# Performance work log

Hardware: AMD Instinct MI355X
Metric: run time of the kernel (lower is better)

## Reference

```python
import jax, jax.numpy as jnp
import numpy as np

B, N, C = 16, 1024, 1024
H = 16            # num_attention_heads
D = C // H        # attention_head_size = 64

def setup_inputs() -> dict:
    key = jax.random.key(0)
    k1, k2, k3 = jax.random.split(key, 3)
    scale = 1.0 / np.sqrt(C)
    return {
        "hidden_states": jax.random.normal(k1, (B, N, C), dtype=jnp.float32),
        "qkv_w": jax.random.normal(k2, (C, 3 * C), dtype=jnp.float32) * scale,
        "qkv_b": jnp.zeros((3 * C,), dtype=jnp.float32),
        "proj_w": jax.random.normal(k3, (C, C), dtype=jnp.float32) * scale,
        "proj_b": jnp.zeros((C,), dtype=jnp.float32),
    }

def reference(hidden_states, qkv_w, qkv_b, proj_w, proj_b):
    # fused QKV projection: [B, N, 3C]
    qkv = hidden_states @ qkv_w + qkv_b
    # reshape to [3, B, H, N, D]
    qkv = qkv.reshape(B, N, 3, H, D).transpose(2, 0, 3, 1, 4)
    q, k, v = qkv[0], qkv[1], qkv[2]
    # attention scores [B, H, N, N]
    scores = jnp.einsum("bhnd,bhmd->bhnm", q, k) / jnp.sqrt(jnp.float32(D))
    probs = jax.nn.softmax(scores, axis=-1)  # dropout_p=0 -> identity
    ctx = jnp.einsum("bhnm,bhmd->bhnd", probs, v)
    ctx = ctx.transpose(0, 2, 1, 3).reshape(B, N, C)
    # output projection
    return ctx @ proj_w + proj_b
```

## Files before the change

### kernel.cpp

```cpp
#include <hip/hip_runtime.h>


#define BB 16
#define NN 1024
#define CC 1024
#define HH 16
#define DD 64
#define BN (BB * NN)
#define HEADELEMS (256 * 1024 * 64)

typedef float  f4     __attribute__((ext_vector_type(4)));
typedef __bf16 bf16x8 __attribute__((ext_vector_type(8)));
typedef __bf16 bf16x4 __attribute__((ext_vector_type(4)));
typedef short  s8v    __attribute__((ext_vector_type(8)));
typedef short  s4v    __attribute__((ext_vector_type(4)));
typedef short  s2v    __attribute__((ext_vector_type(2)));

#if __has_builtin(__builtin_amdgcn_exp2f)
#define EXP2(x) __builtin_amdgcn_exp2f(x)
#else
#define EXP2(x) exp2f(x)
#endif

__device__ __forceinline__ short f2bf(float x) {
  union { float f; unsigned u; } a; a.f = x;
  unsigned r = a.u + 0x7fffu + ((a.u >> 16) & 1u);
  return (short)(r >> 16);
}

__device__ __forceinline__ void gl_lds16(const void* g, void* l) {
  __builtin_amdgcn_global_load_lds((__attribute__((address_space(1))) void*)g,
                                   (__attribute__((address_space(3))) void*)l,
                                   16, 0, 0);
}

__device__ __forceinline__ f4 mfma16(bf16x8 a, bf16x8 b, f4 c) {
  return __builtin_amdgcn_mfma_f32_16x16x32_bf16(a, b, c, 0, 0, 0);
}

__global__ void cast_bf16(const float* __restrict__ x, short* __restrict__ y) {
  int i = (blockIdx.x * 256 + threadIdx.x) * 4;
  float4 v = *(const float4*)&x[i];
  s4v o;
  o[0] = f2bf(v.x); o[1] = f2bf(v.y); o[2] = f2bf(v.z); o[3] = f2bf(v.w);
  *(s4v*)&y[i] = o;
}

__global__ void transpose_cast(const float* __restrict__ W, short* __restrict__ Wt,
                               int K, int Nw) {
  __shared__ float tile[32][33];
  int bx = blockIdx.x, by = blockIdx.y;
  int t = threadIdx.x;
  int tc = t & 31, tr = t >> 5;
#pragma unroll
  for (int i = 0; i < 4; ++i) {
    int r = tr + i * 8;
    tile[r][tc] = W[(size_t)(by * 32 + r) * Nw + bx * 32 + tc];
  }
  __syncthreads();
#pragma unroll
  for (int i = 0; i < 4; ++i) {
    int r = tr + i * 8;
    Wt[(size_t)(bx * 32 + r) * K + by * 32 + tc] = f2bf(tile[tc][r]);
  }
}

#define GSTAGE_A(buf, kb)                                                      \
  {                                                                            \
    _Pragma("unroll")                                                          \
    for (int rblk = 0; rblk < 4; ++rblk) {                                     \
      int rbase = (w * 4 + rblk) * 8;                                          \
      gl_lds16(A + (size_t)(row0 + rbase + sr8) * K + (kb) + sc8 * 8,          \
               &la[buf][rbase * 64]);                                          \
    }                                                                          \
  }
#define GSTAGE_B(buf, kb)                                                      \
  {                                                                            \
    _Pragma("unroll")                                                          \
    for (int bblk = 0; bblk < 2; ++bblk) {                                     \
      int rbase = (w * 2 + bblk) * 8;                                          \
      gl_lds16(Bt + (size_t)(col0 + rbase + sr8) * K + (kb) + sc8 * 8,         \
               &lb[buf][rbase * 64]);                                          \
    }                                                                          \
  }

template <int EPI>
__global__ __launch_bounds__(512, 1)
void gemm_bt(const short* __restrict__ A, const short* __restrict__ Bt,
             const float* __restrict__ bias, float* __restrict__ Cf,
             short* __restrict__ Cq, int M, int N, int K) {
  __shared__ short la[3][256 * 64];
  __shared__ short lb[2][128 * 64];
  const int t = threadIdx.x, lane = t & 63, w = t >> 6;
  int bid = blockIdx.y * gridDim.x + blockIdx.x;
  int xcd = bid & 7, sub = bid >> 3;
  int grp = sub >> 5, rem = sub & 31;
  int xb = grp * 4 + (rem & 3), yb = xcd * 8 + (rem >> 2);
  const int row0 = yb * 256, col0 = xb * 128;
  const int wm = (w >> 1) * 64, wn = (w & 1) * 64;
  const int q = lane >> 4, ln = lane & 15;
  const int sr8 = lane >> 3;
  const int sc8 = (lane & 7) ^ sr8;
  f4 acc[4][4] = {};

  const int NT = K >> 6;
  GSTAGE_A(0, 0);
  GSTAGE_B(0, 0);
  __builtin_amdgcn_sched_barrier(0);
  GSTAGE_A(1, 64);
  asm volatile("s_waitcnt vmcnt(4)" ::: "memory");
  __builtin_amdgcn_s_barrier();
  __builtin_amdgcn_sched_barrier(0);

  int curA = 0;
  for (int tt = 0; tt < NT; ++tt) {
    if (tt + 1 < NT) GSTAGE_B((tt + 1) & 1, (tt + 1) * 64);
    __builtin_amdgcn_sched_barrier(0);
    if (tt + 2 < NT) {
      int a2 = curA + 2; if (a2 >= 3) a2 -= 3;
      GSTAGE_A(a2, (tt + 2) * 64);
    }
    __builtin_amdgcn_sched_barrier(0);
#pragma unroll
    for (int ks2 = 0; ks2 < 2; ++ks2) {
      const int c8 = ks2 * 4 + q;
      const int swz = (c8 ^ (ln & 7)) * 8;
      bf16x8 af[4], bfr[4];
#pragma unroll
      for (int i = 0; i < 4; ++i) {
        af[i]  = *(const bf16x8*)&la[curA][(wm + i * 16 + ln) * 64 + swz];
        bfr[i] = *(const bf16x8*)&lb[tt & 1][(wn + i * 16 + ln) * 64 + swz];
      }
      __builtin_amdgcn_s_setprio(1);
#pragma unroll
      for (int i = 0; i < 4; ++i)
#pragma unroll
        for (int j = 0; j < 4; ++j)
          acc[i][j] = mfma16(af[i], bfr[j], acc[i][j]);
      __builtin_amdgcn_s_setprio(0);
    }
    if (tt + 2 < NT) asm volatile("s_waitcnt vmcnt(4)" ::: "memory");
    else             asm volatile("s_waitcnt vmcnt(0)" ::: "memory");
    __builtin_amdgcn_s_barrier();
    __builtin_amdgcn_sched_barrier(0);
    curA = (curA == 2) ? 0 : curA + 1;
  }

#pragma unroll
  for (int i = 0; i < 4; ++i) {
    int rbase = row0 + wm + i * 16 + q * 4;
#pragma unroll
    for (int j = 0; j < 4; ++j) {
      int col = col0 + wn + j * 16 + ln;
      float bv = bias[col];
      if (EPI == 0) {
#pragma unroll
        for (int r2 = 0; r2 < 4; ++r2)
          Cf[(size_t)(rbase + r2) * N + col] = acc[i][j][r2] + bv;
      } else {
        int which = col >> 10, c = col & 1023;
        int h = c >> 6, d = c & 63;
        if (which == 2) {
          int bh = (rbase >> 10) * HH + h;
          s4v vv;
#pragma unroll
          for (int r2 = 0; r2 < 4; ++r2) vv[r2] = f2bf(acc[i][j][r2] + bv);
          *(s4v*)&Cq[(size_t)2 * HEADELEMS + ((size_t)bh * DD + d) * NN + (rbase & 1023)] = vv;
        } else {
          float scale = (which == 0) ? 0.1803368801f : 1.0f;
#pragma unroll
          for (int r2 = 0; r2 < 4; ++r2) {
            int row = rbase + r2;
            int bh = (row >> 10) * HH + h;
            size_t idx = ((size_t)bh * NN + (row & 1023)) * DD + d;
            Cq[(size_t)which * HEADELEMS + idx] = f2bf((acc[i][j][r2] + bv) * scale);
          }
        }
      }
    }
  }
}

__global__ __launch_bounds__(512, 4)
void attn(const short* __restrict__ Qg, const short* __restrict__ Kg,
          const short* __restrict__ Vtg, short* __restrict__ ctx) {
  __shared__ short sQP[256 * 64];
  __shared__ short sK[2][64 * 64];
  __shared__ short sV[2][64 * 64];
  const int t = threadIdx.x, lane = t & 63, w = t >> 6;
  const int bh = blockIdx.x, qb = blockIdx.y;
  const short* Qh = Qg + (size_t)bh * (NN * DD) + qb * 256 * DD;
  const short* Kh = Kg + (size_t)bh * (NN * DD);
  const short* Vh = Vtg + (size_t)bh * (NN * DD);

#pragma unroll
  for (int k = 0; k < 4; ++k) {
    int i = t + k * 512;
    int r = i >> 3, c = i & 7;
    gl_lds16(Qh + r * DD + ((c ^ (r & 7)) * 8), &sQP[i * 8]);
  }
  const int sr = t >> 3, sc = t & 7;
  const int ssc = ((sc ^ (sr & 7)) * 8);
  gl_lds16(Kh + sr * DD + ssc, &sK[0][t * 8]);
  gl_lds16(Vh + (size_t)sr * NN + ssc, &sV[0][t * 8]);

  __syncthreads();

  const int q = lane >> 4, ln = lane & 15;
  const int wq = w * 32;
  const int sw = ln & 7;

  bf16x8 qf[2][2];
#pragma unroll
  for (int ks = 0; ks < 2; ++ks)
#pragma unroll
    for (int g = 0; g < 2; ++g)
      qf[ks][g] = *(const bf16x8*)&sQP[(wq + g * 16 + ln) * 64 + (((ks * 4 + q) ^ sw) * 8)];

  f4 o[2][4] = {};
  float lsum0 = 0.f, lsum1 = 0.f;

  for (int kt = 0; kt < 16; ++kt) {
    const int cur = kt & 1;
    if (kt < 15) {
      const int nb = cur ^ 1;
      gl_lds16(Kh + (kt + 1) * 64 * DD + sr * DD + ssc, &sK[nb][t * 8]);
      gl_lds16(Vh + (size_t)sr * NN + (kt + 1) * 64 + ssc, &sV[nb][t * 8]);
    }

    f4 s[4][2] = {};
    __builtin_amdgcn_s_setprio(1);
#pragma unroll
    for (int ks = 0; ks < 2; ++ks)
#pragma unroll
      for (int ki = 0; ki < 4; ++ki) {
        bf16x8 kf = *(const bf16x8*)&sK[cur][(ki * 16 + ln) * 64 + (((ks * 4 + q) ^ sw) * 8)];
        s[ki][0] = mfma16(kf, qf[ks][0], s[ki][0]);
        s[ki][1] = mfma16(kf, qf[ks][1], s[ki][1]);
      }
    __builtin_amdgcn_s_setprio(0);

#pragma unroll
    for (int g = 0; g < 2; ++g)
#pragma unroll
      for (int ki = 0; ki < 4; ++ki) {
        f4 sv = s[ki][g];
        float p0 = EXP2(sv[0]), p1 = EXP2(sv[1]);
        float p2 = EXP2(sv[2]), p3 = EXP2(sv[3]);
        if (g == 0) lsum0 += (p0 + p1) + (p2 + p3);
        else        lsum1 += (p0 + p1) + (p2 + p3);
        bf16x4 pk;
        pk[0] = (__bf16)p0; pk[1] = (__bf16)p1;
        pk[2] = (__bf16)p2; pk[3] = (__bf16)p3;
        *(bf16x4*)&sQP[(wq + g * 16 + ln) * 64 +
                       (((2 * ki + (q >> 1)) ^ sw) * 8) + (q & 1) * 4] = pk;
      }

    __builtin_amdgcn_s_setprio(1);
#pragma unroll
    for (int ks = 0; ks < 2; ++ks) {
      bf16x8 vf[4];
#pragma unroll
      for (int j = 0; j < 4; ++j)
        vf[j] = *(const bf16x8*)&sV[cur][(j * 16 + ln) * 64 + (((ks * 4 + q) ^ sw) * 8)];
#pragma unroll
      for (int g = 0; g < 2; ++g) {
        bf16x8 pf = *(const bf16x8*)&sQP[(wq + g * 16 + ln) * 64 + (((ks * 4 + q) ^ sw) * 8)];
#pragma unroll
        for (int j = 0; j < 4; ++j)
          o[g][j] = mfma16(pf, vf[j], o[g][j]);
      }
    }
    __builtin_amdgcn_s_setprio(0);

    __syncthreads();
  }

#pragma unroll
  for (int g = 0; g < 2; ++g) {
    float lfull = (g == 0) ? lsum0 : lsum1;
    lfull += __shfl_xor(lfull, 16);
    lfull += __shfl_xor(lfull, 32);
#pragma unroll
    for (int r = 0; r < 4; ++r) {
      float lr = __shfl(lfull, q * 4 + r);
      float inv = 1.0f / lr;
      int token_row = qb * 256 + wq + g * 16 + q * 4 + r;
      size_t base = ((size_t)(bh >> 4) * NN + token_row) * CC + (bh & 15) * DD;
#pragma unroll
      for (int j = 0; j < 4; ++j)
        ctx[base + j * 16 + ln] = f2bf(o[g][j][r] * inv);
    }
  }
}

extern "C" void kernel_launch(void* const* d_in, const int* in_sizes, int n_in,
                              void* d_out, int out_size, void* d_ws, size_t ws_size,
                              hipStream_t stream) {
  const float* hs     = (const float*)d_in[0];
  const float* qkv_w  = (const float*)d_in[1];
  const float* qkv_b  = (const float*)d_in[2];
  const float* proj_w = (const float*)d_in[3];
  const float* proj_b = (const float*)d_in[4];

  short* ws = (short*)d_ws;
  if (ws_size < 176160768ull) return;
  short* Xbf = ws;
  short* Wq  = ws + 16777216;
  short* Wp  = ws + 19922944;
  short* Qm  = ws + 20971520;
  short* Km  = ws + 37748736;
  short* Vt  = ws + 54525952;
  short* Ctx = ws + 71303168;

  cast_bf16<<<16384, 256, 0, stream>>>(hs, Xbf);
  transpose_cast<<<dim3(96, 32), 256, 0, stream>>>(qkv_w, Wq, 1024, 3072);
  transpose_cast<<<dim3(32, 32), 256, 0, stream>>>(proj_w, Wp, 1024, 1024);

  gemm_bt<1><<<dim3(24, 64), 512, 0, stream>>>(Xbf, Wq, qkv_b, nullptr, Qm,
                                               BN, 3 * CC, CC);
  attn<<<dim3(256, 4), 512, 0, stream>>>(Qm, Km, Vt, Ctx);
  gemm_bt<0><<<dim3(8, 64), 512, 0, stream>>>(Ctx, Wp, proj_b, (float*)d_out, nullptr,
                                              BN, CC, CC);
}
```

Before: 409.0 us.

## Split GEMM k-step into two half-phases and compute softmax row sums via MFMA

The GEMM main loop is split into two half-K phases. Each phase loads its fragments from LDS, then issues one of the next global stages (B in the first, A in the second), then barriers before its MFMAs, so global loads are interleaved with compute rather than all issued up front. In the attention kernel, the softmax denominator is now accumulated by an extra MFMA of the bf16 probabilities against a ones vector. This replaces the scalar adds and cross-lane shuffles. The sum now uses the bf16-rounded probabilities, which matches what is fed to the PV product, and it adds extra barriers and MFMA work in exchange.

New measurement: 391.3 us. 4.3% less time.

```diff
diff --git a/kernel.cpp b/kernel.cpp
--- a/kernel.cpp
+++ b/kernel.cpp
@@ -114,23 +114,17 @@
 
   int curA = 0;
   for (int tt = 0; tt < NT; ++tt) {
-    if (tt + 1 < NT) GSTAGE_B((tt + 1) & 1, (tt + 1) * 64);
-    __builtin_amdgcn_sched_barrier(0);
-    if (tt + 2 < NT) {
-      int a2 = curA + 2; if (a2 >= 3) a2 -= 3;
-      GSTAGE_A(a2, (tt + 2) * 64);
-    }
-    __builtin_amdgcn_sched_barrier(0);
-#pragma unroll
-    for (int ks2 = 0; ks2 < 2; ++ks2) {
-      const int c8 = ks2 * 4 + q;
-      const int swz = (c8 ^ (ln & 7)) * 8;
+    {
+      const int swz = (q ^ (ln & 7)) * 8;
       bf16x8 af[4], bfr[4];
 #pragma unroll
       for (int i = 0; i < 4; ++i) {
         af[i]  = *(const bf16x8*)&la[curA][(wm + i * 16 + ln) * 64 + swz];
         bfr[i] = *(const bf16x8*)&lb[tt & 1][(wn + i * 16 + ln) * 64 + swz];
       }
+      if (tt + 1 < NT) GSTAGE_B((tt + 1) & 1, (tt + 1) * 64);
+      __builtin_amdgcn_s_barrier();
+      __builtin_amdgcn_sched_barrier(0);
       __builtin_amdgcn_s_setprio(1);
 #pragma unroll
       for (int i = 0; i < 4; ++i)
@@ -138,12 +132,36 @@
         for (int j = 0; j < 4; ++j)
           acc[i][j] = mfma16(af[i], bfr[j], acc[i][j]);
       __builtin_amdgcn_s_setprio(0);
-    }
-    if (tt + 2 < NT) asm volatile("s_waitcnt vmcnt(4)" ::: "memory");
-    else             asm volatile("s_waitcnt vmcnt(0)" ::: "memory");
-    __builtin_amdgcn_s_barrier();
-    __builtin_amdgcn_sched_barrier(0);
-    curA = (curA == 2) ? 0 : curA + 1;
+      __builtin_amdgcn_s_barrier();
+      __builtin_amdgcn_sched_barrier(0);
+    }
+    {
+      const int swz = ((4 + q) ^ (ln & 7)) * 8;
+      bf16x8 af[4], bfr[4];
+#pragma unroll
+      for (int i = 0; i < 4; ++i) {
+        af[i]  = *(const bf16x8*)&la[curA][(wm + i * 16 + ln) * 64 + swz];
+        bfr[i] = *(const bf16x8*)&lb[tt & 1][(wn + i * 16 + ln) * 64 + swz];
+      }
+      if (tt + 2 < NT) {
+        int a2 = curA + 2; if (a2 >= 3) a2 -= 3;
+        GSTAGE_A(a2, (tt + 2) * 64);
+      }
+      __builtin_amdgcn_s_barrier();
+      __builtin_amdgcn_sched_barrier(0);
+      __builtin_amdgcn_s_setprio(1);
+#pragma unroll
+      for (int i = 0; i < 4; ++i)
+#pragma unroll
+        for (int j = 0; j < 4; ++j)
+          acc[i][j] = mfma16(af[i], bfr[j], acc[i][j]);
+      __builtin_amdgcn_s_setprio(0);
+      if (tt + 2 < NT) asm volatile("s_waitcnt vmcnt(4)" ::: "memory");
+      else             asm volatile("s_waitcnt vmcnt(0)" ::: "memory");
+      __builtin_amdgcn_s_barrier();
+      __builtin_amdgcn_sched_barrier(0);
+      curA = (curA == 2) ? 0 : curA + 1;
+    }
   }
 
 #pragma unroll
@@ -217,8 +235,12 @@
     for (int g = 0; g < 2; ++g)
       qf[ks][g] = *(const bf16x8*)&sQP[(wq + g * 16 + ln) * 64 + (((ks * 4 + q) ^ sw) * 8)];
 
+  bf16x8 onesb;
+#pragma unroll
+  for (int j = 0; j < 8; ++j) onesb[j] = (__bf16)1.0f;
+
   f4 o[2][4] = {};
-  float lsum0 = 0.f, lsum1 = 0.f;
+  f4 l4[2] = {};
 
   for (int kt = 0; kt < 16; ++kt) {
     const int cur = kt & 1;
@@ -245,13 +267,9 @@
 #pragma unroll
       for (int ki = 0; ki < 4; ++ki) {
         f4 sv = s[ki][g];
-        float p0 = EXP2(sv[0]), p1 = EXP2(sv[1]);
-        float p2 = EXP2(sv[2]), p3 = EXP2(sv[3]);
-        if (g == 0) lsum0 += (p0 + p1) + (p2 + p3);
-        else        lsum1 += (p0 + p1) + (p2 + p3);
         bf16x4 pk;
-        pk[0] = (__bf16)p0; pk[1] = (__bf16)p1;
-        pk[2] = (__bf16)p2; pk[3] = (__bf16)p3;
+        pk[0] = (__bf16)EXP2(sv[0]); pk[1] = (__bf16)EXP2(sv[1]);
+        pk[2] = (__bf16)EXP2(sv[2]); pk[3] = (__bf16)EXP2(sv[3]);
         *(bf16x4*)&sQP[(wq + g * 16 + ln) * 64 +
                        (((2 * ki + (q >> 1)) ^ sw) * 8) + (q & 1) * 4] = pk;
       }
@@ -266,6 +284,7 @@
 #pragma unroll
       for (int g = 0; g < 2; ++g) {
         bf16x8 pf = *(const bf16x8*)&sQP[(wq + g * 16 + ln) * 64 + (((ks * 4 + q) ^ sw) * 8)];
+        l4[g] = mfma16(pf, onesb, l4[g]);
 #pragma unroll
         for (int j = 0; j < 4; ++j)
           o[g][j] = mfma16(pf, vf[j], o[g][j]);
@@ -277,21 +296,16 @@
   }
 
 #pragma unroll
-  for (int g = 0; g < 2; ++g) {
-    float lfull = (g == 0) ? lsum0 : lsum1;
-    lfull += __shfl_xor(lfull, 16);
-    lfull += __shfl_xor(lfull, 32);
+  for (int g = 0; g < 2; ++g)
 #pragma unroll
     for (int r = 0; r < 4; ++r) {
-      float lr = __shfl(lfull, q * 4 + r);
-      float inv = 1.0f / lr;
+      float inv = 1.0f / l4[g][r];
       int token_row = qb * 256 + wq + g * 16 + q * 4 + r;
       size_t base = ((size_t)(bh >> 4) * NN + token_row) * CC + (bh & 15) * DD;
 #pragma unroll
       for (int j = 0; j < 4; ++j)
         ctx[base + j * 16 + ln] = f2bf(o[g][j][r] * inv);
     }
-  }
 }
 
 extern "C" void kernel_launch(void* const* d_in, const int* in_sizes, int n_in,
```
